# Optimization experiments

Measured on AMD Instinct MI355X. Metric: run time of the kernel, lower is better.

Reference implementation:

```python
import jax, jax.numpy as jnp
import numpy as np

N = 100000
E = 3200000
D_IN = 256
D_HID = 256
D_OUT = 128
EPS = 1e-12


def setup_inputs() -> dict:
    key = jax.random.key(0)
    ks = jax.random.split(key, 8)
    x = jax.random.normal(ks[0], (N, D_IN), dtype=jnp.float32)
    edge_src = jax.random.randint(ks[1], (E,), 0, N, dtype=jnp.int32)
    edge_dst = jax.random.randint(ks[2], (E,), 0, N, dtype=jnp.int32)
    # mean aggregation: each row of the sparse adj sums to 1 -> val = 1/deg(src row)
    deg = jax.ops.segment_sum(jnp.ones((E,), jnp.float32), edge_src, num_segments=N)
    edge_val = 1.0 / jnp.maximum(deg, 1.0)[edge_src]
    # Xavier-uniform linear weights (torch Linear: y = x @ W.T + b); store as [in, out]
    def xavier(k, fan_in, fan_out):
        lim = jnp.sqrt(6.0 / (fan_in + fan_out))
        return jax.random.uniform(k, (fan_in, fan_out), jnp.float32, -lim, lim)
    W1 = xavier(ks[3], 2 * D_IN, D_HID)
    b1 = jnp.zeros((D_HID,), jnp.float32)
    W2 = xavier(ks[4], 2 * D_HID, D_OUT)
    b2 = jnp.zeros((D_OUT,), jnp.float32)
    return {"x": x, "edge_src": edge_src, "edge_dst": edge_dst, "edge_val": edge_val,
            "W1": W1, "b1": b1, "W2": W2, "b2": b2}


def _sage_layer(feat, edge_src, edge_dst, edge_val, W, b):
    # spmm: out[i] = sum_j adj[i,j] * feat[j]  (COO rows=edge_src, cols=edge_dst)
    msg = feat[edge_dst] * edge_val[:, None]              # [E, d]
    neigh = jax.ops.segment_sum(msg, edge_src, num_segments=feat.shape[0])  # [N, d]
    combined = jnp.concatenate([feat, neigh], axis=1) @ W + b  # [N, d_out]
    # F.normalize(p=2, dim=1): x / max(||x||_2, eps)
    norm = jnp.sqrt(jnp.sum(combined * combined, axis=1, keepdims=True))
    return combined / jnp.maximum(norm, EPS)


def reference(x, edge_src, edge_dst, edge_val, W1, b1, W2, b2):
    h = _sage_layer(x, edge_src, edge_dst, edge_val, W1, b1)
    h = jax.nn.relu(h)
    # dropout is identity at inference (training=False)
    return _sage_layer(h, edge_src, edge_dst, edge_val, W2, b2)
```

## Files before the change

### kernel.cpp

```cpp
#include <hip/hip_runtime.h>


#define N_NODES 100000
#define N_EDGES 3200000
#define DF      256

typedef __bf16 bf16x8 __attribute__((ext_vector_type(8)));
typedef float  f32x4  __attribute__((ext_vector_type(4)));
typedef float  f32x2  __attribute__((ext_vector_type(2)));

__device__ __forceinline__ ushort f2bf(float f){
  uint u = __float_as_uint(f);
  u += 0x7fffu + ((u >> 16) & 1u);
  return (ushort)(u >> 16);
}
__device__ __forceinline__ float bflo(uint u){ return __uint_as_float(u << 16); }
__device__ __forceinline__ float bfhi(uint u){ return __uint_as_float(u & 0xffff0000u); }
__device__ __forceinline__ float bfs(ushort u){ return __uint_as_float((uint)u << 16); }


__global__ void k_hist(const int* __restrict__ src, int* __restrict__ deg, int E){
  int i = blockIdx.x * blockDim.x + threadIdx.x;
  if(i < E) atomicAdd(&deg[src[i]], 1);
}

__global__ void k_scan1(const int* __restrict__ deg, int* __restrict__ rowptr,
                        int* __restrict__ partials, int n){
  __shared__ int s[256];
  const int t = threadIdx.x;
  const int base = blockIdx.x * 1024 + t * 4;
  int v[4], run[4];
  #pragma unroll
  for(int j = 0; j < 4; j++) v[j] = (base + j < n) ? deg[base + j] : 0;
  int sum = 0;
  #pragma unroll
  for(int j = 0; j < 4; j++){ run[j] = sum; sum += v[j]; }
  s[t] = sum;
  __syncthreads();
  for(int off = 1; off < 256; off <<= 1){
    int x = (t >= off) ? s[t - off] : 0;
    __syncthreads();
    s[t] += x;
    __syncthreads();
  }
  const int texcl = s[t] - sum;
  #pragma unroll
  for(int j = 0; j < 4; j++) if(base + j < n) rowptr[base + j] = texcl + run[j];
  if(t == 255) partials[blockIdx.x] = s[255];
}

__global__ void k_scan2(int* __restrict__ partials, int nb,
                        int* __restrict__ rowptr, int n, int E){
  __shared__ int s[128];
  const int t = threadIdx.x;
  int v = (t < nb) ? partials[t] : 0;
  s[t] = v;
  __syncthreads();
  for(int off = 1; off < 128; off <<= 1){
    int x = (t >= off) ? s[t - off] : 0;
    __syncthreads();
    s[t] += x;
    __syncthreads();
  }
  if(t < nb) partials[t] = s[t] - v;
  if(t == 0) rowptr[n] = E;
}

__global__ void k_scan3(int* __restrict__ rowptr, const int* __restrict__ partials, int n){
  int i = blockIdx.x * blockDim.x + threadIdx.x;
  if(i < n) rowptr[i] += partials[i >> 10];
}

__global__ void k_fill(const int* __restrict__ src, const int* __restrict__ dst,
                       const int* __restrict__ rowptr, int* __restrict__ cursor,
                       int* __restrict__ col, int E){
  int i = blockIdx.x * blockDim.x + threadIdx.x;
  if(i < E){
    int r = src[i];
    int p = atomicAdd(&cursor[r], 1);
    col[rowptr[r] + p] = dst[i];
  }
}


__global__ void k_cvt(const float4* __restrict__ x4, uint4* __restrict__ outb,
                      uint2* __restrict__ outq, int n8,
                      int* __restrict__ za, int* __restrict__ zb, int nz){
  int i = blockIdx.x * blockDim.x + threadIdx.x;
  if(i < nz){ za[i] = 0; zb[i] = 0; }
  if(i >= n8) return;
  const float4 p = x4[2*i], q = x4[2*i+1];
  uint4 o;
  o.x = (uint)f2bf(p.x) | ((uint)f2bf(p.y) << 16);
  o.y = (uint)f2bf(p.z) | ((uint)f2bf(p.w) << 16);
  o.z = (uint)f2bf(q.x) | ((uint)f2bf(q.y) << 16);
  o.w = (uint)f2bf(q.z) | ((uint)f2bf(q.w) << 16);
  outb[i] = o;
  uint w0 = __builtin_amdgcn_cvt_pk_fp8_f32(p.x, p.y, 0u, false);
  w0      = __builtin_amdgcn_cvt_pk_fp8_f32(p.z, p.w, w0, true);
  uint w1 = __builtin_amdgcn_cvt_pk_fp8_f32(q.x, q.y, 0u, false);
  w1      = __builtin_amdgcn_cvt_pk_fp8_f32(q.z, q.w, w1, true);
  outq[i] = make_uint2(w0, w1);
}


template<int DOUT>
__global__ void k_packw(const float* __restrict__ W, uint4* __restrict__ Wp,
                        int ksteps, int krow0){
  constexpr int NT = DOUT / 16;
  const int tid = blockIdx.x * blockDim.x + threadIdx.x;
  if(tid >= NT * ksteps * 64) return;
  const int l   = tid & 63;
  const int s   = (tid >> 6) % ksteps;
  const int n   = tid / (64 * ksteps);
  const int grp = l >> 4, li = l & 15;
  const int col = n * 16 + li;
  ushort b[8];
  #pragma unroll
  for(int i = 0; i < 8; i++){
    const int k = krow0 + s * 32 + grp * 8 + i;
    b[i] = f2bf(W[(size_t)k * DOUT + col]);
  }
  uint4 o;
  o.x = (uint)b[0] | ((uint)b[1] << 16);
  o.y = (uint)b[2] | ((uint)b[3] << 16);
  o.z = (uint)b[4] | ((uint)b[5] << 16);
  o.w = (uint)b[6] | ((uint)b[7] << 16);
  Wp[tid] = o;
}


__global__ __launch_bounds__(256)
void k_gather_q(const uchar* __restrict__ xq, const int* __restrict__ rowptr,
                const int* __restrict__ colidx, ushort* __restrict__ nbuf, int Nn){
  const int node = (blockIdx.x * blockDim.x + threadIdx.x) >> 6;
  const int lane = threadIdx.x & 63;
  if(node >= Nn) return;
  const int half = lane >> 4;
  const int li   = lane & 15;
  const int s0 = rowptr[node];
  const int s1 = rowptr[node + 1];
  const float invd = (s1 > s0) ? (1.0f / (float)(s1 - s0)) : 0.0f;
  const uint cmax = (uint)(Nn - 1);
  float a[16];
  #pragma unroll
  for(int i = 0; i < 16; i++) a[i] = 0.f;

  #define DECODE_ACC(v)                                                        \
    {                                                                          \
      const uint uu[4] = {(v).x, (v).y, (v).z, (v).w};                         \
      _Pragma("unroll")                                                        \
      for(int m = 0; m < 4; m++){                                              \
        f32x2 lo = __builtin_amdgcn_cvt_pk_f32_fp8(uu[m], false);              \
        f32x2 hi = __builtin_amdgcn_cvt_pk_f32_fp8(uu[m], true);               \
        a[m*4+0] += lo.x; a[m*4+1] += lo.y;                                    \
        a[m*4+2] += hi.x; a[m*4+3] += hi.y;                                    \
      }                                                                        \
    }

  int e = s0;
  for(; e + 16 <= s1; e += 16){
    uint c[4];
    #pragma unroll
    for(int j = 0; j < 4; j++) c[j] = min((uint)colidx[e + j * 4 + half], cmax);
    uint4 v[4];
    #pragma unroll
    for(int j = 0; j < 4; j++) v[j] = *(const uint4*)(xq + (size_t)c[j] * 256 + li * 16);
    #pragma unroll
    for(int j = 0; j < 4; j++) DECODE_ACC(v[j]);
  }
  for(; e + 4 <= s1; e += 4){
    const uint c = min((uint)colidx[e + half], cmax);
    const uint4 v = *(const uint4*)(xq + (size_t)c * 256 + li * 16);
    DECODE_ACC(v);
  }
  if(half < s1 - e){
    const uint c = min((uint)colidx[e + half], cmax);
    const uint4 v = *(const uint4*)(xq + (size_t)c * 256 + li * 16);
    DECODE_ACC(v);
  }
  #undef DECODE_ACC

  #pragma unroll
  for(int i = 0; i < 16; i++){
    a[i] += __shfl_xor(a[i], 16);
    a[i] += __shfl_xor(a[i], 32);
  }
  if(lane < 16){
    uint4 o1, o2;
    o1.x = (uint)f2bf(a[ 0]*invd) | ((uint)f2bf(a[ 1]*invd) << 16);
    o1.y = (uint)f2bf(a[ 2]*invd) | ((uint)f2bf(a[ 3]*invd) << 16);
    o1.z = (uint)f2bf(a[ 4]*invd) | ((uint)f2bf(a[ 5]*invd) << 16);
    o1.w = (uint)f2bf(a[ 6]*invd) | ((uint)f2bf(a[ 7]*invd) << 16);
    o2.x = (uint)f2bf(a[ 8]*invd) | ((uint)f2bf(a[ 9]*invd) << 16);
    o2.y = (uint)f2bf(a[10]*invd) | ((uint)f2bf(a[11]*invd) << 16);
    o2.z = (uint)f2bf(a[12]*invd) | ((uint)f2bf(a[13]*invd) << 16);
    o2.w = (uint)f2bf(a[14]*invd) | ((uint)f2bf(a[15]*invd) << 16);
    ushort* p = nbuf + (size_t)node * DF + li * 16;
    *(uint4*)(p)     = o1;
    *(uint4*)(p + 8) = o2;
  }
}


template<int DIMV>
__global__ __launch_bounds__(256)
void k_gather_b(const ushort* __restrict__ xb, const int* __restrict__ rowptr,
                const int* __restrict__ colidx, ushort* __restrict__ nbuf, int Nn){
  constexpr int LPR = DIMV / 8;
  constexpr int EPG = 64 / LPR;
  const int node = (blockIdx.x * blockDim.x + threadIdx.x) >> 6;
  const int lane = threadIdx.x & 63;
  if(node >= Nn) return;
  const int half = lane / LPR;
  const int li   = lane % LPR;
  const int s0 = rowptr[node];
  const int s1 = rowptr[node + 1];
  const float invd = (s1 > s0) ? (1.0f / (float)(s1 - s0)) : 0.0f;
  const uint cmax = (uint)(Nn - 1);
  float a[8] = {0.f,0.f,0.f,0.f,0.f,0.f,0.f,0.f};
  int e = s0;
  for(; e + 4 * EPG <= s1; e += 4 * EPG){
    uint c[4];
    #pragma unroll
    for(int j = 0; j < 4; j++) c[j] = min((uint)colidx[e + j * EPG + half], cmax);
    uint4 v[4];
    #pragma unroll
    for(int j = 0; j < 4; j++) v[j] = *(const uint4*)(xb + (size_t)c[j] * DIMV + li * 8);
    #pragma unroll
    for(int j = 0; j < 4; j++){
      a[0] += bflo(v[j].x); a[1] += bfhi(v[j].x);
      a[2] += bflo(v[j].y); a[3] += bfhi(v[j].y);
      a[4] += bflo(v[j].z); a[5] += bfhi(v[j].z);
      a[6] += bflo(v[j].w); a[7] += bfhi(v[j].w);
    }
  }
  for(; e + EPG <= s1; e += EPG){
    const uint c = min((uint)colidx[e + half], cmax);
    const uint4 v = *(const uint4*)(xb + (size_t)c * DIMV + li * 8);
    a[0] += bflo(v.x); a[1] += bfhi(v.x);
    a[2] += bflo(v.y); a[3] += bfhi(v.y);
    a[4] += bflo(v.z); a[5] += bfhi(v.z);
    a[6] += bflo(v.w); a[7] += bfhi(v.w);
  }
  if(half < s1 - e){
    const uint c = min((uint)colidx[e + half], cmax);
    const uint4 v = *(const uint4*)(xb + (size_t)c * DIMV + li * 8);
    a[0] += bflo(v.x); a[1] += bfhi(v.x);
    a[2] += bflo(v.y); a[3] += bfhi(v.y);
    a[4] += bflo(v.z); a[5] += bfhi(v.z);
    a[6] += bflo(v.w); a[7] += bfhi(v.w);
  }
  #pragma unroll
  for(int off = LPR; off < 64; off <<= 1)
    #pragma unroll
    for(int i = 0; i < 8; i++) a[i] += __shfl_xor(a[i], off);
  if(lane < LPR){
    uint4 o;
    o.x = (uint)f2bf(a[0]*invd) | ((uint)f2bf(a[1]*invd) << 16);
    o.y = (uint)f2bf(a[2]*invd) | ((uint)f2bf(a[3]*invd) << 16);
    o.z = (uint)f2bf(a[4]*invd) | ((uint)f2bf(a[5]*invd) << 16);
    o.w = (uint)f2bf(a[6]*invd) | ((uint)f2bf(a[7]*invd) << 16);
    *(uint4*)(nbuf + (size_t)node * DIMV + li * 8) = o;
  }
}


template<int DOUT, int KS, bool TWOSRC, bool ADDG, bool RELU, bool NORM, bool OUTBF16>
__launch_bounds__(256, 2)
__global__ void k_mlp(const ushort* __restrict__ A0, const ushort* __restrict__ A1,
                      const uint4* __restrict__ Wp, const float* __restrict__ bias,
                      const ushort* __restrict__ g,
                      ushort* __restrict__ outb, float* __restrict__ outf, int Nn)
{
  constexpr int NT   = DOUT / 16;
  constexpr int DIMA = TWOSRC ? KS * 16 : KS * 32;
  const int l     = threadIdx.x & 63;
  const int w     = threadIdx.x >> 6;
  const int nodeb = blockIdx.x * 64 + w * 16;
  const int grp   = l >> 4;
  const int li    = l & 15;

  const int rowL = min(nodeb + li, Nn - 1);
  uint4 a[KS];
  if(TWOSRC){
    const ushort* xr = A0 + (size_t)rowL * DIMA;
    const ushort* nr = A1 + (size_t)rowL * DIMA;
    #pragma unroll
    for(int s = 0; s < KS/2; s++) a[s]        = *(const uint4*)(xr + s * 32 + grp * 8);
    #pragma unroll
    for(int s = 0; s < KS/2; s++) a[s + KS/2] = *(const uint4*)(nr + s * 32 + grp * 8);
  } else {
    const ushort* xr = A0 + (size_t)rowL * DIMA;
    #pragma unroll
    for(int s = 0; s < KS; s++) a[s] = *(const uint4*)(xr + s * 32 + grp * 8);
  }

  f32x4 acc[NT];
  #pragma unroll
  for(int n = 0; n < NT; n++){
    f32x4 c = {0.f, 0.f, 0.f, 0.f};
    #pragma unroll
    for(int s = 0; s < KS; s++){
      const uint4 b = Wp[(size_t)(n * KS + s) * 64 + l];
      c = __builtin_amdgcn_mfma_f32_16x16x32_bf16(
            __builtin_bit_cast(bf16x8, a[s]),
            __builtin_bit_cast(bf16x8, b), c, 0, 0, 0);
    }
    acc[n] = c;
  }

  if(NORM){
    #pragma unroll
    for(int n = 0; n < NT; n++){
      const float bv = bias[n * 16 + li];
      acc[n][0] += bv; acc[n][1] += bv; acc[n][2] += bv; acc[n][3] += bv;
    }
  }

  if(ADDG){
    #pragma unroll
    for(int r = 0; r < 4; r++){
      const int rowg = min(nodeb + grp * 4 + r, Nn - 1);
      #pragma unroll
      for(int n = 0; n < NT; n++)
        acc[n][r] += bfs(g[(size_t)rowg * DOUT + n * 16 + li]);
    }
  }

  float rn[4] = {1.f, 1.f, 1.f, 1.f};
  if(NORM){
    #pragma unroll
    for(int r = 0; r < 4; r++){
      float ss = 0.f;
      #pragma unroll
      for(int n = 0; n < NT; n++) ss = fmaf(acc[n][r], acc[n][r], ss);
      ss += __shfl_xor(ss, 1);
      ss += __shfl_xor(ss, 2);
      ss += __shfl_xor(ss, 4);
      ss += __shfl_xor(ss, 8);
      rn[r] = 1.0f / fmaxf(sqrtf(ss), 1e-12f);
    }
  }

  #pragma unroll
  for(int r = 0; r < 4; r++){
    const int node = nodeb + grp * 4 + r;
    if(node < Nn){
      #pragma unroll
      for(int n = 0; n < NT; n++){
        float y = acc[n][r];
        if(NORM) y *= rn[r];
        if(RELU) y = fmaxf(y, 0.0f);
        const size_t idx = (size_t)node * DOUT + n * 16 + li;
        if(OUTBF16) outb[idx] = f2bf(y);
        else        outf[idx] = y;
      }
    }
  }
}


extern "C" void kernel_launch(void* const* d_in, const int* in_sizes, int n_in,
                              void* d_out, int out_size, void* d_ws, size_t ws_size,
                              hipStream_t stream) {
  const float* x    = (const float*)d_in[0];
  const int*   esrc = (const int*)  d_in[1];
  const int*   edst = (const int*)  d_in[2];
  const float* W1   = (const float*)d_in[4];
  const float* b1   = (const float*)d_in[5];
  const float* W2   = (const float*)d_in[6];
  const float* b2   = (const float*)d_in[7];
  float* out = (float*)d_out;

  const int N = N_NODES, E = N_EDGES;

  char* ws = (char*)d_ws;
  size_t off = 0;
  auto alloc = [&](size_t bytes) -> void* {
    void* p = ws + off;
    off += (bytes + 255) & ~(size_t)255;
    return p;
  };
  int*    deg      = (int*)   alloc((size_t)N * 4);
  int*    rowptr   = (int*)   alloc((size_t)(N + 1) * 4);
  int*    cursor   = (int*)   alloc((size_t)N * 4);
  int*    partials = (int*)   alloc(512);
  int*    colidx   = (int*)   alloc((size_t)E * 4);
  ushort* xbuf     = (ushort*)alloc((size_t)N * DF * 2);
  uchar*  xq       = (uchar*) alloc((size_t)N * DF);
  ushort* hbuf     = (ushort*)alloc((size_t)N * DF * 2);
  ushort* nbuf     = (ushort*)alloc((size_t)N * DF * 2);
  uint4*  Wp1      = (uint4*) alloc((size_t)16 * 16 * 64 * 16);
  uint4*  Wp2a     = (uint4*) alloc((size_t) 8 *  8 * 64 * 16);
  uint4*  Wp2b     = (uint4*) alloc((size_t) 8 *  8 * 64 * 16);
  if(off > ws_size) return;

  ushort* Pb = nbuf;
  ushort* gb = nbuf + (size_t)N * 128;

  const int NBLK_SCAN = (N + 1023) / 1024;
  const int n8 = N * DF / 8;

  k_cvt<<<(n8 + 255) / 256, 256, 0, stream>>>((const float4*)x, (uint4*)xbuf,
                                              (uint2*)xq, n8, deg, cursor, N);
  k_packw<256><<<(16 * 16 * 64 + 255) / 256, 256, 0, stream>>>(W1,  Wp1, 16, 0);
  k_packw<128><<<( 8 *  8 * 64 + 255) / 256, 256, 0, stream>>>(W2, Wp2a,  8, 0);
  k_packw<128><<<( 8 *  8 * 64 + 255) / 256, 256, 0, stream>>>(W2, Wp2b,  8, 256);

  k_hist <<<(E + 255) / 256, 256, 0, stream>>>(esrc, deg, E);
  k_scan1<<<NBLK_SCAN,       256, 0, stream>>>(deg, rowptr, partials, N);
  k_scan2<<<1,               128, 0, stream>>>(partials, NBLK_SCAN, rowptr, N, E);
  k_scan3<<<(N + 255) / 256, 256, 0, stream>>>(rowptr, partials, N);
  k_fill <<<(E + 255) / 256, 256, 0, stream>>>(esrc, edst, rowptr, cursor, colidx, E);

  const int GRID_MLP = (N + 63) / 64;

  k_gather_q<<<N / 4, 256, 0, stream>>>(xq, rowptr, colidx, nbuf, N);
  k_mlp<256, 16, true, false, true, true, true>
      <<<GRID_MLP, 256, 0, stream>>>(xbuf, nbuf, Wp1, b1, nullptr, hbuf, nullptr, N);

  k_mlp<128, 8, false, false, false, false, true>
      <<<GRID_MLP, 256, 0, stream>>>(hbuf, nullptr, Wp2b, nullptr, nullptr, Pb, nullptr, N);
  k_gather_b<128><<<N / 4, 256, 0, stream>>>(Pb, rowptr, colidx, gb, N);
  k_mlp<128, 8, false, true, false, true, false>
      <<<GRID_MLP, 256, 0, stream>>>(hbuf, nullptr, Wp2a, b2, gb, nullptr, out, N);
}
```

Measured before the change: 677.2 us.

## Bucket CSR fill through LDS and gather layer-2 projections in fp8

```diff
diff --git a/kernel.cpp b/kernel.cpp
--- a/kernel.cpp
+++ b/kernel.cpp
@@ -4,6 +4,7 @@
 #define N_NODES 100000
 #define N_EDGES 3200000
 #define DF      256
+#define NBUCK   ((N_NODES + 63) / 64)
 
 typedef __bf16 bf16x8 __attribute__((ext_vector_type(8)));
 typedef float  f32x4  __attribute__((ext_vector_type(4)));
@@ -16,12 +17,11 @@
 }
 __device__ __forceinline__ float bflo(uint u){ return __uint_as_float(u << 16); }
 __device__ __forceinline__ float bfhi(uint u){ return __uint_as_float(u & 0xffff0000u); }
-__device__ __forceinline__ float bfs(ushort u){ return __uint_as_float((uint)u << 16); }
 
 
 __global__ void k_hist(const int* __restrict__ src, int* __restrict__ deg, int E){
   int i = blockIdx.x * blockDim.x + threadIdx.x;
-  if(i < E) atomicAdd(&deg[src[i]], 1);
+  if(i < E) atomicAdd(&deg[__builtin_nontemporal_load(&src[i])], 1);
 }
 
 __global__ void k_scan1(const int* __restrict__ deg, int* __restrict__ rowptr,
@@ -71,23 +71,47 @@
   if(i < n) rowptr[i] += partials[i >> 10];
 }
 
-__global__ void k_fill(const int* __restrict__ src, const int* __restrict__ dst,
-                       const int* __restrict__ rowptr, int* __restrict__ cursor,
-                       int* __restrict__ col, int E){
+__global__ void k_bucket(const int* __restrict__ esrc, const int* __restrict__ edst,
+                         const int* __restrict__ rowptr, int* __restrict__ bcur,
+                         uint* __restrict__ bq, int E){
   int i = blockIdx.x * blockDim.x + threadIdx.x;
   if(i < E){
-    int r = src[i];
-    int p = atomicAdd(&cursor[r], 1);
-    col[rowptr[r] + p] = dst[i];
+    const int s = __builtin_nontemporal_load(&esrc[i]);
+    const int d = __builtin_nontemporal_load(&edst[i]);
+    const int base = rowptr[s & ~63];
+    const int p = atomicAdd(&bcur[s >> 6], 1);
+    bq[base + p] = (uint)d | ((uint)(s & 63) << 17);
+  }
+}
+
+__global__ __launch_bounds__(256)
+void k_fillb(const uint* __restrict__ bq, const int* __restrict__ rowptr,
+             int* __restrict__ colidx, int Nn){
+  __shared__ int rp[65];
+  __shared__ int lcur[64];
+  const int t  = threadIdx.x;
+  const int r0 = blockIdx.x << 6;
+  if(t < 65) rp[t] = rowptr[min(r0 + t, Nn)];
+  if(t < 64) lcur[t] = 0;
+  __syncthreads();
+  const int base = rp[0];
+  const int cnt  = rp[min(64, Nn - r0)] - base;
+  for(int e = t; e < cnt; e += 256){
+    const uint w = __builtin_nontemporal_load(&bq[base + e]);
+    const int li = (int)(w >> 17);
+    const int d  = (int)(w & 0x1FFFFu);
+    const int p  = atomicAdd(&lcur[li], 1);
+    colidx[rp[li] + p] = d;
   }
 }
 
 
 __global__ void k_cvt(const float4* __restrict__ x4, uint4* __restrict__ outb,
                       uint2* __restrict__ outq, int n8,
-                      int* __restrict__ za, int* __restrict__ zb, int nz){
+                      int* __restrict__ za, int nza, int* __restrict__ zb, int nzb){
   int i = blockIdx.x * blockDim.x + threadIdx.x;
-  if(i < nz){ za[i] = 0; zb[i] = 0; }
+  if(i < nza) za[i] = 0;
+  if(i < nzb) zb[i] = 0;
   if(i >= n8) return;
   const float4 p = x4[2*i], q = x4[2*i+1];
   uint4 o;
@@ -130,14 +154,17 @@
 }
 
 
+template<int RB>
 __global__ __launch_bounds__(256)
 void k_gather_q(const uchar* __restrict__ xq, const int* __restrict__ rowptr,
                 const int* __restrict__ colidx, ushort* __restrict__ nbuf, int Nn){
+  constexpr int LPR = RB / 16;
+  constexpr int EPG = 64 / LPR;
   const int node = (blockIdx.x * blockDim.x + threadIdx.x) >> 6;
   const int lane = threadIdx.x & 63;
   if(node >= Nn) return;
-  const int half = lane >> 4;
-  const int li   = lane & 15;
+  const int half = lane / LPR;
+  const int li   = lane % LPR;
   const int s0 = rowptr[node];
   const int s1 = rowptr[node + 1];
   const float invd = (s1 > s0) ? (1.0f / (float)(s1 - s0)) : 0.0f;
@@ -159,34 +186,35 @@
     }
 
   int e = s0;
-  for(; e + 16 <= s1; e += 16){
+  for(; e + 4 * EPG <= s1; e += 4 * EPG){
     uint c[4];
     #pragma unroll
-    for(int j = 0; j < 4; j++) c[j] = min((uint)colidx[e + j * 4 + half], cmax);
+    for(int j = 0; j < 4; j++)
+      c[j] = min((uint)__builtin_nontemporal_load(&colidx[e + j * EPG + half]), cmax);
     uint4 v[4];
     #pragma unroll
-    for(int j = 0; j < 4; j++) v[j] = *(const uint4*)(xq + (size_t)c[j] * 256 + li * 16);
+    for(int j = 0; j < 4; j++) v[j] = *(const uint4*)(xq + (size_t)c[j] * RB + li * 16);
     #pragma unroll
     for(int j = 0; j < 4; j++) DECODE_ACC(v[j]);
   }
-  for(; e + 4 <= s1; e += 4){
-    const uint c = min((uint)colidx[e + half], cmax);
-    const uint4 v = *(const uint4*)(xq + (size_t)c * 256 + li * 16);
+  for(; e + EPG <= s1; e += EPG){
+    const uint c = min((uint)__builtin_nontemporal_load(&colidx[e + half]), cmax);
+    const uint4 v = *(const uint4*)(xq + (size_t)c * RB + li * 16);
     DECODE_ACC(v);
   }
   if(half < s1 - e){
-    const uint c = min((uint)colidx[e + half], cmax);
-    const uint4 v = *(const uint4*)(xq + (size_t)c * 256 + li * 16);
+    const uint c = min((uint)__builtin_nontemporal_load(&colidx[e + half]), cmax);
+    const uint4 v = *(const uint4*)(xq + (size_t)c * RB + li * 16);
     DECODE_ACC(v);
   }
   #undef DECODE_ACC
 
   #pragma unroll
-  for(int i = 0; i < 16; i++){
-    a[i] += __shfl_xor(a[i], 16);
-    a[i] += __shfl_xor(a[i], 32);
-  }
-  if(lane < 16){
+  for(int off = LPR; off < 64; off <<= 1)
+    #pragma unroll
+    for(int i = 0; i < 16; i++) a[i] += __shfl_xor(a[i], off);
+
+  if(lane < LPR){
     uint4 o1, o2;
     o1.x = (uint)f2bf(a[ 0]*invd) | ((uint)f2bf(a[ 1]*invd) << 16);
     o1.y = (uint)f2bf(a[ 2]*invd) | ((uint)f2bf(a[ 3]*invd) << 16);
@@ -196,82 +224,19 @@
     o2.y = (uint)f2bf(a[10]*invd) | ((uint)f2bf(a[11]*invd) << 16);
     o2.z = (uint)f2bf(a[12]*invd) | ((uint)f2bf(a[13]*invd) << 16);
     o2.w = (uint)f2bf(a[14]*invd) | ((uint)f2bf(a[15]*invd) << 16);
-    ushort* p = nbuf + (size_t)node * DF + li * 16;
+    ushort* p = nbuf + (size_t)node * RB + li * 16;
     *(uint4*)(p)     = o1;
     *(uint4*)(p + 8) = o2;
   }
 }
 
 
-template<int DIMV>
-__global__ __launch_bounds__(256)
-void k_gather_b(const ushort* __restrict__ xb, const int* __restrict__ rowptr,
-                const int* __restrict__ colidx, ushort* __restrict__ nbuf, int Nn){
-  constexpr int LPR = DIMV / 8;
-  constexpr int EPG = 64 / LPR;
-  const int node = (blockIdx.x * blockDim.x + threadIdx.x) >> 6;
-  const int lane = threadIdx.x & 63;
-  if(node >= Nn) return;
-  const int half = lane / LPR;
-  const int li   = lane % LPR;
-  const int s0 = rowptr[node];
-  const int s1 = rowptr[node + 1];
-  const float invd = (s1 > s0) ? (1.0f / (float)(s1 - s0)) : 0.0f;
-  const uint cmax = (uint)(Nn - 1);
-  float a[8] = {0.f,0.f,0.f,0.f,0.f,0.f,0.f,0.f};
-  int e = s0;
-  for(; e + 4 * EPG <= s1; e += 4 * EPG){
-    uint c[4];
-    #pragma unroll
-    for(int j = 0; j < 4; j++) c[j] = min((uint)colidx[e + j * EPG + half], cmax);
-    uint4 v[4];
-    #pragma unroll
-    for(int j = 0; j < 4; j++) v[j] = *(const uint4*)(xb + (size_t)c[j] * DIMV + li * 8);
-    #pragma unroll
-    for(int j = 0; j < 4; j++){
-      a[0] += bflo(v[j].x); a[1] += bfhi(v[j].x);
-      a[2] += bflo(v[j].y); a[3] += bfhi(v[j].y);
-      a[4] += bflo(v[j].z); a[5] += bfhi(v[j].z);
-      a[6] += bflo(v[j].w); a[7] += bfhi(v[j].w);
-    }
-  }
-  for(; e + EPG <= s1; e += EPG){
-    const uint c = min((uint)colidx[e + half], cmax);
-    const uint4 v = *(const uint4*)(xb + (size_t)c * DIMV + li * 8);
-    a[0] += bflo(v.x); a[1] += bfhi(v.x);
-    a[2] += bflo(v.y); a[3] += bfhi(v.y);
-    a[4] += bflo(v.z); a[5] += bfhi(v.z);
-    a[6] += bflo(v.w); a[7] += bfhi(v.w);
-  }
-  if(half < s1 - e){
-    const uint c = min((uint)colidx[e + half], cmax);
-    const uint4 v = *(const uint4*)(xb + (size_t)c * DIMV + li * 8);
-    a[0] += bflo(v.x); a[1] += bfhi(v.x);
-    a[2] += bflo(v.y); a[3] += bfhi(v.y);
-    a[4] += bflo(v.z); a[5] += bfhi(v.z);
-    a[6] += bflo(v.w); a[7] += bfhi(v.w);
-  }
-  #pragma unroll
-  for(int off = LPR; off < 64; off <<= 1)
-    #pragma unroll
-    for(int i = 0; i < 8; i++) a[i] += __shfl_xor(a[i], off);
-  if(lane < LPR){
-    uint4 o;
-    o.x = (uint)f2bf(a[0]*invd) | ((uint)f2bf(a[1]*invd) << 16);
-    o.y = (uint)f2bf(a[2]*invd) | ((uint)f2bf(a[3]*invd) << 16);
-    o.z = (uint)f2bf(a[4]*invd) | ((uint)f2bf(a[5]*invd) << 16);
-    o.w = (uint)f2bf(a[6]*invd) | ((uint)f2bf(a[7]*invd) << 16);
-    *(uint4*)(nbuf + (size_t)node * DIMV + li * 8) = o;
-  }
-}
-
-
-template<int DOUT, int KS, bool TWOSRC, bool ADDG, bool RELU, bool NORM, bool OUTBF16>
+template<int DOUT, int KS, bool TWOSRC, bool ADDG, bool RELU, bool NORM, int OMODE>
 __launch_bounds__(256, 2)
 __global__ void k_mlp(const ushort* __restrict__ A0, const ushort* __restrict__ A1,
                       const uint4* __restrict__ Wp, const float* __restrict__ bias,
                       const ushort* __restrict__ g,
-                      ushort* __restrict__ outb, float* __restrict__ outf, int Nn)
+                      void* __restrict__ outp, int Nn)
 {
   constexpr int NT   = DOUT / 16;
   constexpr int DIMA = TWOSRC ? KS * 16 : KS * 32;
@@ -322,9 +287,11 @@
     #pragma unroll
     for(int r = 0; r < 4; r++){
       const int rowg = min(nodeb + grp * 4 + r, Nn - 1);
-      #pragma unroll
-      for(int n = 0; n < NT; n++)
-        acc[n][r] += bfs(g[(size_t)rowg * DOUT + n * 16 + li]);
+      const uint4 gv = *(const uint4*)(g + (size_t)rowg * DOUT + li * 8);
+      acc[0][r] += bflo(gv.x); acc[1][r] += bfhi(gv.x);
+      acc[2][r] += bflo(gv.y); acc[3][r] += bfhi(gv.y);
+      acc[4][r] += bflo(gv.z); acc[5][r] += bfhi(gv.z);
+      acc[6][r] += bflo(gv.w); acc[7][r] += bfhi(gv.w);
     }
   }
 
@@ -347,14 +314,22 @@
   for(int r = 0; r < 4; r++){
     const int node = nodeb + grp * 4 + r;
     if(node < Nn){
-      #pragma unroll
-      for(int n = 0; n < NT; n++){
-        float y = acc[n][r];
-        if(NORM) y *= rn[r];
-        if(RELU) y = fmaxf(y, 0.0f);
-        const size_t idx = (size_t)node * DOUT + n * 16 + li;
-        if(OUTBF16) outb[idx] = f2bf(y);
-        else        outf[idx] = y;
+      if(OMODE == 2){
+        uint w0 = __builtin_amdgcn_cvt_pk_fp8_f32(acc[0][r], acc[1][r], 0u, false);
+        w0      = __builtin_amdgcn_cvt_pk_fp8_f32(acc[2][r], acc[3][r], w0, true);
+        uint w1 = __builtin_amdgcn_cvt_pk_fp8_f32(acc[4][r], acc[5][r], 0u, false);
+        w1      = __builtin_amdgcn_cvt_pk_fp8_f32(acc[6][r], acc[7][r], w1, true);
+        *(uint2*)((uchar*)outp + (size_t)node * DOUT + li * 8) = make_uint2(w0, w1);
+      } else {
+        #pragma unroll
+        for(int n = 0; n < NT; n++){
+          float y = acc[n][r];
+          if(NORM) y *= rn[r];
+          if(RELU) y = fmaxf(y, 0.0f);
+          const size_t idx = (size_t)node * DOUT + n * 16 + li;
+          if(OMODE == 1) ((ushort*)outp)[idx] = f2bf(y);
+          else           ((float*)outp)[idx]  = y;
+        }
       }
     }
   }
@@ -384,9 +359,10 @@
   };
   int*    deg      = (int*)   alloc((size_t)N * 4);
   int*    rowptr   = (int*)   alloc((size_t)(N + 1) * 4);
-  int*    cursor   = (int*)   alloc((size_t)N * 4);
+  int*    bcur     = (int*)   alloc((size_t)NBUCK * 4);
   int*    partials = (int*)   alloc(512);
   int*    colidx   = (int*)   alloc((size_t)E * 4);
+  uint*   bq       = (uint*)  alloc((size_t)E * 4);
   ushort* xbuf     = (ushort*)alloc((size_t)N * DF * 2);
   uchar*  xq       = (uchar*) alloc((size_t)N * DF);
   ushort* hbuf     = (ushort*)alloc((size_t)N * DF * 2);
@@ -396,33 +372,34 @@
   uint4*  Wp2b     = (uint4*) alloc((size_t) 8 *  8 * 64 * 16);
   if(off > ws_size) return;
 
-  ushort* Pb = nbuf;
-  ushort* gb = nbuf + (size_t)N * 128;
+  uchar*  Pq = (uchar*)nbuf;
+  ushort* gb = nbuf + (size_t)N * 64;
 
   const int NBLK_SCAN = (N + 1023) / 1024;
   const int n8 = N * DF / 8;
 
   k_cvt<<<(n8 + 255) / 256, 256, 0, stream>>>((const float4*)x, (uint4*)xbuf,
-                                              (uint2*)xq, n8, deg, cursor, N);
+                                              (uint2*)xq, n8, deg, N, bcur, NBUCK);
   k_packw<256><<<(16 * 16 * 64 + 255) / 256, 256, 0, stream>>>(W1,  Wp1, 16, 0);
   k_packw<128><<<( 8 *  8 * 64 + 255) / 256, 256, 0, stream>>>(W2, Wp2a,  8, 0);
   k_packw<128><<<( 8 *  8 * 64 + 255) / 256, 256, 0, stream>>>(W2, Wp2b,  8, 256);
 
-  k_hist <<<(E + 255) / 256, 256, 0, stream>>>(esrc, deg, E);
-  k_scan1<<<NBLK_SCAN,       256, 0, stream>>>(deg, rowptr, partials, N);
-  k_scan2<<<1,               128, 0, stream>>>(partials, NBLK_SCAN, rowptr, N, E);
-  k_scan3<<<(N + 255) / 256, 256, 0, stream>>>(rowptr, partials, N);
-  k_fill <<<(E + 255) / 256, 256, 0, stream>>>(esrc, edst, rowptr, cursor, colidx, E);
+  k_hist  <<<(E + 255) / 256, 256, 0, stream>>>(esrc, deg, E);
+  k_scan1 <<<NBLK_SCAN,       256, 0, stream>>>(deg, rowptr, partials, N);
+  k_scan2 <<<1,               128, 0, stream>>>(partials, NBLK_SCAN, rowptr, N, E);
+  k_scan3 <<<(N + 255) / 256, 256, 0, stream>>>(rowptr, partials, N);
+  k_bucket<<<(E + 255) / 256, 256, 0, stream>>>(esrc, edst, rowptr, bcur, bq, E);
+  k_fillb <<<NBUCK,           256, 0, stream>>>(bq, rowptr, colidx, N);
 
   const int GRID_MLP = (N + 63) / 64;
 
-  k_gather_q<<<N / 4, 256, 0, stream>>>(xq, rowptr, colidx, nbuf, N);
-  k_mlp<256, 16, true, false, true, true, true>
-      <<<GRID_MLP, 256, 0, stream>>>(xbuf, nbuf, Wp1, b1, nullptr, hbuf, nullptr, N);
-
-  k_mlp<128, 8, false, false, false, false, true>
-      <<<GRID_MLP, 256, 0, stream>>>(hbuf, nullptr, Wp2b, nullptr, nullptr, Pb, nullptr, N);
-  k_gather_b<128><<<N / 4, 256, 0, stream>>>(Pb, rowptr, colidx, gb, N);
-  k_mlp<128, 8, false, true, false, true, false>
-      <<<GRID_MLP, 256, 0, stream>>>(hbuf, nullptr, Wp2a, b2, gb, nullptr, out, N);
-}
+  k_gather_q<256><<<N / 4, 256, 0, stream>>>(xq, rowptr, colidx, nbuf, N);
+  k_mlp<256, 16, true, false, true, true, 1>
+      <<<GRID_MLP, 256, 0, stream>>>(xbuf, nbuf, Wp1, b1, nullptr, hbuf, N);
+
+  k_mlp<128, 8, false, false, false, false, 2>
+      <<<GRID_MLP, 256, 0, stream>>>(hbuf, nullptr, Wp2b, nullptr, nullptr, Pq, N);
+  k_gather_q<128><<<N / 4, 256, 0, stream>>>(Pq, rowptr, colidx, gb, N);
+  k_mlp<128, 8, false, true, false, true, 0>
+      <<<GRID_MLP, 256, 0, stream>>>(hbuf, nullptr, Wp2a, b2, gb, out, N);
+}
```

Result: slower. 1.018 ms (+50.3%).
